# Kernel tuning notes

Hardware: AMD Instinct MI355X
Metric: run time of the kernel (lower is better)

The kernel has to match this reference:

```python
import jax, jax.numpy as jnp
import numpy as np


def setup_inputs() -> dict:
    key = jax.random.key(0)
    k1, k2 = jax.random.split(key)
    B, C, H, W = 8, 128, 192, 256
    a = jax.random.normal(k1, (B, C, H, W), dtype=jnp.float32)
    b = jax.random.normal(k2, (B, C, H, W), dtype=jnp.float32)
    return {"a": a, "b": b, "max_displacement": 40}


def reference(a, b, max_displacement):
    """Horizontal correlation cost volume.

    out[:, ctr, h, w] = sum_c a[:, c, h, w] * b[:, c, h, w - (D - ctr)]
    for ctr in 0..D (out-of-range b treated as zero), matching the torch
    shift-and-pad loop over displacements i = -D..0.
    """
    D = max_displacement
    W = a.shape[-1]
    # Pad b once on the left by D; then the shifted slice for index ctr is
    # bp[..., ctr:ctr+W]  (static slices -> jit-friendly, no big stack kept).
    bp = jnp.pad(b, ((0, 0), (0, 0), (0, 0), (D, 0)))
    outs = [jnp.einsum('bchw,bchw->bhw', a, bp[..., ctr:ctr + W])
            for ctr in range(D + 1)]  # small fixed loop over D+1 displacements
    return jnp.stack(outs, axis=1)  # [B, D+1, H, W]
```

## Files before the change

kernel.cpp:

```cpp
#include <hip/hip_runtime.h>

constexpr int Bsz  = 8;
constexpr int Cch  = 128;
constexpr int Hh   = 192;
constexpr int Ww   = 256;
constexpr int Dmax = 40;
constexpr int NC   = Dmax + 1;

constexpr int CC     = 16;
constexpr int NCHUNK = Cch / CC;
constexpr int LBW    = 304;
constexpr int WT     = 4;
constexpr int CT     = 12;


__global__ __launch_bounds__(256, 4)
void corr_kernel(const float* __restrict__ A, const float* __restrict__ B,
                 float* __restrict__ O) {
    __shared__ __align__(16) float a_lds[CC * Ww];
    __shared__ __align__(16) float b_lds[CC * LBW];

    const int tid = threadIdx.x;
    const int row = blockIdx.x;
    const int bb  = row / Hh;
    const int h   = row - bb * Hh;

    const int wg   = tid & 63;
    const int g    = tid >> 6;
    const int ctr0 = g * CT;
    const int w0   = wg * WT;

    for (int i = tid; i < CC * 48; i += 256) {
        int c = i / 48, j = i - c * 48;
        int jj = (j < 40) ? j : (256 + j);
        b_lds[c * LBW + jj] = 0.0f;
    }

    float acc[CT][WT];
#pragma unroll
    for (int k = 0; k < CT; ++k)
#pragma unroll
        for (int j = 0; j < WT; ++j) acc[k][j] = 0.0f;

    const float* arow = A + ((size_t)bb * Cch * Hh + h) * Ww;
    const float* brow = B + ((size_t)bb * Cch * Hh + h) * Ww;

    for (int chunk = 0; chunk < NCHUNK; ++chunk) {
        __syncthreads();
        const int c0 = chunk * CC;
#pragma unroll
        for (int it = 0; it < 4; ++it) {
            int idx = it * 256 + tid;
            int ci  = idx >> 6;
            int wq  = idx & 63;
            const float4 av = *(const float4*)(arow + (size_t)(c0 + ci) * (Hh * Ww) + wq * 4);
            const float4 bv = *(const float4*)(brow + (size_t)(c0 + ci) * (Hh * Ww) + wq * 4);
            *(float4*)(a_lds + ci * Ww + wq * 4)        = av;
            *(float4*)(b_lds + ci * LBW + 40 + wq * 4)  = bv;
        }
        __syncthreads();

#pragma unroll
        for (int c = 0; c < CC; ++c) {
            float av[4];
            *(float4*)av = *(const float4*)(a_lds + c * Ww + w0);
            float bq[16];
            const float* bp = b_lds + c * LBW + w0 + ctr0;
            *(float4*)(bq + 0)  = *(const float4*)(bp + 0);
            *(float4*)(bq + 4)  = *(const float4*)(bp + 4);
            *(float4*)(bq + 8)  = *(const float4*)(bp + 8);
            *(float4*)(bq + 12) = *(const float4*)(bp + 12);
#pragma unroll
            for (int k = 0; k < CT; ++k)
#pragma unroll
                for (int j = 0; j < WT; ++j)
                    acc[k][j] = fmaf(av[j], bq[k + j], acc[k][j]);
        }
    }

#pragma unroll
    for (int k = 0; k < CT; ++k) {
        int ctr = ctr0 + k;
        if (ctr < NC) {
            float4 v = make_float4(acc[k][0], acc[k][1], acc[k][2], acc[k][3]);
            *(float4*)(O + (((size_t)bb * NC + ctr) * Hh + h) * Ww + w0) = v;
        }
    }
}

extern "C" void kernel_launch(void* const* d_in, const int* in_sizes, int n_in,
                              void* d_out, int out_size, void* d_ws, size_t ws_size,
                              hipStream_t stream) {
    const float* a = (const float*)d_in[0];
    const float* b = (const float*)d_in[1];
    float* out = (float*)d_out;
    dim3 grid(Bsz * Hh);
    dim3 block(256);
    corr_kernel<<<grid, block, 0, stream>>>(a, b, out);
}
```

Measured before the change: 491.3 us.

## Compute correlation with bf16 MFMA band tiles instead of fp32 FMA

Rewrites the per-row correlation as small bf16 matrix multiplies using 16x16x32 MFMA. A and B are converted to bf16 and transposed into LDS, and each wave computes 16x16 blocks of the w-by-u product; only the diagonal band inside the displacement range is kept. Results are staged through LDS so the global stores are coalesced. This computes redundant off-band products and lowers input precision to bf16, which risks accuracy tolerance failures.

```diff
diff --git a/kernel.cpp b/kernel.cpp
--- a/kernel.cpp
+++ b/kernel.cpp
@@ -1,90 +1,116 @@
 #include <hip/hip_runtime.h>
 
-constexpr int Bsz  = 8;
-constexpr int Cch  = 128;
-constexpr int Hh   = 192;
-constexpr int Ww   = 256;
-constexpr int Dmax = 40;
-constexpr int NC   = Dmax + 1;
 
-constexpr int CC     = 16;
-constexpr int NCHUNK = Cch / CC;
-constexpr int LBW    = 304;
-constexpr int WT     = 4;
-constexpr int CT     = 12;
+constexpr int Bsz = 8, Cch = 128, Hh = 192, Ww = 256, NC = 41;
+constexpr int CHW = Hh * Ww;
+constexpr int LDB = 40;
+constexpr int A_BYTES = 256 * LDB * 2;
+constexpr int OSTRIDE = 260;
 
+using short8  = __attribute__((ext_vector_type(8))) short;
+using floatx4 = __attribute__((ext_vector_type(4))) float;
 
-__global__ __launch_bounds__(256, 4)
-void corr_kernel(const float* __restrict__ A, const float* __restrict__ B,
-                 float* __restrict__ O) {
-    __shared__ __align__(16) float a_lds[CC * Ww];
-    __shared__ __align__(16) float b_lds[CC * LBW];
+__device__ inline unsigned short f2bf(float x) {
+    unsigned int u = __float_as_uint(x);
+    u += 0x7fffu + ((u >> 16) & 1u);
+    return (unsigned short)(u >> 16);
+}
 
-    const int tid = threadIdx.x;
-    const int row = blockIdx.x;
-    const int bb  = row / Hh;
-    const int h   = row - bb * Hh;
+__global__ __launch_bounds__(256, 3)
+void corr_mfma(const float* __restrict__ A, const float* __restrict__ B,
+               float* __restrict__ O) {
+    __shared__ __align__(16) unsigned char smem[44800];
+    unsigned short* aT   = (unsigned short*)smem;
+    unsigned short* bT   = (unsigned short*)(smem + A_BYTES);
+    float*          outp = (float*)smem;
 
-    const int wg   = tid & 63;
-    const int g    = tid >> 6;
-    const int ctr0 = g * CT;
-    const int w0   = wg * WT;
+    const int tid  = threadIdx.x;
+    const int lane = tid & 63, wave = tid >> 6;
+    const int row  = blockIdx.x;
+    const int bb   = row / Hh, h = row - bb * Hh;
 
-    for (int i = tid; i < CC * 48; i += 256) {
-        int c = i / 48, j = i - c * 48;
-        int jj = (j < 40) ? j : (256 + j);
-        b_lds[c * LBW + jj] = 0.0f;
-    }
+    const float* base_a = A + (size_t)bb * Cch * CHW + (size_t)h * Ww;
+    const float* base_b = B + (size_t)bb * Cch * CHW + (size_t)h * Ww;
 
-    float acc[CT][WT];
+    const int c8 = tid & 3;
+    const int w4 = tid >> 2;
+    const int wi = lane & 15, kg = lane >> 4;
+
+    floatx4 acc[4][4];
 #pragma unroll
-    for (int k = 0; k < CT; ++k)
+    for (int i = 0; i < 4; ++i)
 #pragma unroll
-        for (int j = 0; j < WT; ++j) acc[k][j] = 0.0f;
+        for (int j = 0; j < 4; ++j) acc[i][j] = (floatx4)0.0f;
 
-    const float* arow = A + ((size_t)bb * Cch * Hh + h) * Ww;
-    const float* brow = B + ((size_t)bb * Cch * Hh + h) * Ww;
-
-    for (int chunk = 0; chunk < NCHUNK; ++chunk) {
+    for (int c0 = 0; c0 < Cch; c0 += 32) {
         __syncthreads();
-        const int c0 = chunk * CC;
+        if (tid < 160) {
+            int u = tid >> 2, cz = (tid & 3) * 8;
+            *(short8*)(bT + u * LDB + cz) = (short8)0;
+        }
+        {
+            float4 la[8];
 #pragma unroll
-        for (int it = 0; it < 4; ++it) {
-            int idx = it * 256 + tid;
-            int ci  = idx >> 6;
-            int wq  = idx & 63;
-            const float4 av = *(const float4*)(arow + (size_t)(c0 + ci) * (Hh * Ww) + wq * 4);
-            const float4 bv = *(const float4*)(brow + (size_t)(c0 + ci) * (Hh * Ww) + wq * 4);
-            *(float4*)(a_lds + ci * Ww + wq * 4)        = av;
-            *(float4*)(b_lds + ci * LBW + 40 + wq * 4)  = bv;
+            for (int i = 0; i < 8; ++i)
+                la[i] = *(const float4*)(base_a + (size_t)(c0 + c8 * 8 + i) * CHW + w4 * 4);
+            const float* laf = (const float*)la;
+#pragma unroll
+            for (int r = 0; r < 4; ++r) {
+                short8 s;
+#pragma unroll
+                for (int i = 0; i < 8; ++i) s[i] = (short)f2bf(laf[i * 4 + r]);
+                *(short8*)(aT + (w4 * 4 + r) * LDB + c8 * 8) = s;
+            }
+        }
+        {
+            float4 lb[8];
+#pragma unroll
+            for (int i = 0; i < 8; ++i)
+                lb[i] = *(const float4*)(base_b + (size_t)(c0 + c8 * 8 + i) * CHW + w4 * 4);
+            const float* lbf = (const float*)lb;
+#pragma unroll
+            for (int r = 0; r < 4; ++r) {
+                short8 s;
+#pragma unroll
+                for (int i = 0; i < 8; ++i) s[i] = (short)f2bf(lbf[i * 4 + r]);
+                *(short8*)(bT + (40 + w4 * 4 + r) * LDB + c8 * 8) = s;
+            }
         }
         __syncthreads();
 
 #pragma unroll
-        for (int c = 0; c < CC; ++c) {
-            float av[4];
-            *(float4*)av = *(const float4*)(a_lds + c * Ww + w0);
-            float bq[16];
-            const float* bp = b_lds + c * LBW + w0 + ctr0;
-            *(float4*)(bq + 0)  = *(const float4*)(bp + 0);
-            *(float4*)(bq + 4)  = *(const float4*)(bp + 4);
-            *(float4*)(bq + 8)  = *(const float4*)(bp + 8);
-            *(float4*)(bq + 12) = *(const float4*)(bp + 12);
+        for (int i = 0; i < 4; ++i) {
+            const int w0 = wave * 64 + i * 16;
+            short8 afrag_a = *(const short8*)(aT + (w0 + wi) * LDB + kg * 8);
 #pragma unroll
-            for (int k = 0; k < CT; ++k)
-#pragma unroll
-                for (int j = 0; j < WT; ++j)
-                    acc[k][j] = fmaf(av[j], bq[k + j], acc[k][j]);
+            for (int j = 0; j < 4; ++j) {
+                const int u0 = w0 + 16 * j;
+                short8 bfrag_b = *(const short8*)(bT + (u0 + wi) * LDB + kg * 8);
+                acc[i][j] = __builtin_amdgcn_mfma_f32_16x16x32_bf16(bfrag_b, afrag_a,
+                                                                    acc[i][j], 0, 0, 0);
+            }
         }
     }
 
+    __syncthreads();
 #pragma unroll
-    for (int k = 0; k < CT; ++k) {
-        int ctr = ctr0 + k;
-        if (ctr < NC) {
-            float4 v = make_float4(acc[k][0], acc[k][1], acc[k][2], acc[k][3]);
-            *(float4*)(O + (((size_t)bb * NC + ctr) * Hh + h) * Ww + w0) = v;
+    for (int i = 0; i < 4; ++i) {
+        const int w0 = wave * 64 + i * 16;
+#pragma unroll
+        for (int j = 0; j < 4; ++j) {
+#pragma unroll
+            for (int r = 0; r < 4; ++r) {
+                int ctr = 16 * j + (kg * 4 + r) - wi;
+                if ((unsigned)ctr <= 40u) outp[ctr * OSTRIDE + w0 + wi] = acc[i][j][r];
+            }
         }
+    }
+    __syncthreads();
+    float* obase = O + ((size_t)bb * NC * Hh + (size_t)h) * Ww;
+    for (int idx = tid; idx < NC * 64; idx += 256) {
+        int ctr = idx >> 6, q = idx & 63;
+        float4 v = *(const float4*)(outp + ctr * OSTRIDE + q * 4);
+        *(float4*)(obase + (size_t)ctr * CHW + q * 4) = v;
     }
 }
 
@@ -94,7 +120,5 @@
     const float* a = (const float*)d_in[0];
     const float* b = (const float*)d_in[1];
     float* out = (float*)d_out;
-    dim3 grid(Bsz * Hh);
-    dim3 block(256);
-    corr_kernel<<<grid, block, 0, stream>>>(a, b, out);
+    corr_mfma<<<dim3(Bsz * Hh), dim3(256), 0, stream>>>(a, b, out);
 }
```

Result: faster. 411.9 us (-16.2%).
